# Kernel tuning notes

Hardware: AMD Instinct MI355X
Metric: run time of the kernel (lower is better)

Reference implementation:

```python
import jax, jax.numpy as jnp
import numpy as np

HID = 256      # hidden_dim
EXPAND = 2
D_INNER = HID * EXPAND
LN_EPS = 1e-5


def _gru(xs, W_ih, W_hh, b_ih, b_hh):
    """torch nn.GRU (batch_first) over axis 1. xs: (N, P, d_inner) -> (N, P, H).
    Gate order (torch): r, z, n."""
    N = xs.shape[0]
    Hd = W_hh.shape[0]
    gi = xs @ W_ih + b_ih                 # (N, P, 3H) - input gates precomputed
    gi = jnp.swapaxes(gi, 0, 1)           # (P, N, 3H) for scan over P
    h0 = jnp.zeros((N, Hd), xs.dtype)

    def step(h, gi_t):
        gh = h @ W_hh + b_hh              # (N, 3H)
        ir, iz, i_n = jnp.split(gi_t, 3, axis=-1)
        hr, hz, h_n = jnp.split(gh, 3, axis=-1)
        r = jax.nn.sigmoid(ir + hr)
        z = jax.nn.sigmoid(iz + hz)
        n = jnp.tanh(i_n + r * h_n)
        h = (1.0 - z) * n + z * h
        return h, h

    _, ys = jax.lax.scan(step, h0, gi)    # (P, N, H)
    return jnp.swapaxes(ys, 0, 1)


def _branch(x2d, lin_W, lin_b, W_ih, W_hh, b_ih, b_hh):
    # Linear -> exact GELU (torch nn.GELU default) -> GRU
    h = jax.nn.gelu(x2d @ lin_W + lin_b, approximate=False)
    return _gru(h, W_ih, W_hh, b_ih, b_hh)


def setup_inputs() -> dict:
    key = jax.random.key(0)
    ks = jax.random.split(key, 16)
    s = 0.05
    p = {
        "x": jax.random.normal(ks[0], (8, 16, 1024, HID), jnp.float32),
        "fwd_lin_W": jax.random.normal(ks[1], (HID, D_INNER)) * s,
        "fwd_lin_b": jnp.zeros((D_INNER,)),
        "fwd_W_ih": jax.random.normal(ks[2], (D_INNER, 3 * HID)) * s,
        "fwd_W_hh": jax.random.normal(ks[3], (HID, 3 * HID)) * s,
        "fwd_b_ih": jnp.zeros((3 * HID,)),
        "fwd_b_hh": jnp.zeros((3 * HID,)),
        "bwd_lin_W": jax.random.normal(ks[4], (HID, D_INNER)) * s,
        "bwd_lin_b": jnp.zeros((D_INNER,)),
        "bwd_W_ih": jax.random.normal(ks[5], (D_INNER, 3 * HID)) * s,
        "bwd_W_hh": jax.random.normal(ks[6], (HID, 3 * HID)) * s,
        "bwd_b_ih": jnp.zeros((3 * HID,)),
        "bwd_b_hh": jnp.zeros((3 * HID,)),
        "proj_W": jax.random.normal(ks[7], (2 * HID, HID)) * s,
        "proj_b": jnp.zeros((HID,)),
        "ln_g": jnp.ones((HID,)),
        "ln_b": jnp.zeros((HID,)),
    }
    return p


def reference(x, fwd_lin_W, fwd_lin_b, fwd_W_ih, fwd_W_hh, fwd_b_ih, fwd_b_hh,
              bwd_lin_W, bwd_lin_b, bwd_W_ih, bwd_W_hh, bwd_b_ih, bwd_b_hh,
              proj_W, proj_b, ln_g, ln_b):
    B, T, P, H = x.shape
    xf = x.reshape(B * T, P, H)  # every timestep gets the identical spatial pass
    f_out = _branch(xf, fwd_lin_W, fwd_lin_b, fwd_W_ih, fwd_W_hh, fwd_b_ih, fwd_b_hh)
    b_out = _branch(xf[:, ::-1], bwd_lin_W, bwd_lin_b, bwd_W_ih, bwd_W_hh, bwd_b_ih, bwd_b_hh)[:, ::-1]
    cat = jnp.concatenate([f_out, b_out], axis=-1)          # (BT, P, 2H)
    out = cat @ proj_W + proj_b                              # (BT, P, H)
    out = out.reshape(B, T, P, H) + x                        # residual
    mu = out.mean(-1, keepdims=True)
    var = out.var(-1, keepdims=True)
    return (out - mu) * jax.lax.rsqrt(var + LN_EPS) * ln_g + ln_b
```

## Files before the change

### kernel.cpp

```cpp
#include <hip/hip_runtime.h>
#include <cmath>


typedef _Float16 h8  __attribute__((ext_vector_type(8)));
typedef float    f32x4 __attribute__((ext_vector_type(4)));

#define MTOT 131072L
#define PSEQ 1024

__device__ __forceinline__ float fast_sigmoid(float x) {
    float e = __builtin_amdgcn_exp2f(-1.44269504089f * x);
    return __builtin_amdgcn_rcpf(1.f + e);
}
__device__ __forceinline__ float fast_tanh(float x) {
    float e = __builtin_amdgcn_exp2f(-2.88539008178f * x);
    return (1.f - e) * __builtin_amdgcn_rcpf(1.f + e);
}

__device__ __forceinline__ void gl_lds16(const void* g, void* lds_wave_base, int lane) {
#if defined(__has_builtin) && __has_builtin(__builtin_amdgcn_global_load_lds)
    __builtin_amdgcn_global_load_lds(
        (const __attribute__((address_space(1))) void*)g,
        (__attribute__((address_space(3))) void*)lds_wave_base, 16, 0, 0);
#else
    *((h8*)lds_wave_base + lane) = *(const h8*)g;
#endif
}

template <int MODE>
__global__ __launch_bounds__(256) void k_gemm2(
    const void* __restrict__ Aa_, const void* __restrict__ Ab_,
    const _Float16* __restrict__ Bt, const float* __restrict__ bias,
    const float* __restrict__ xres, void* __restrict__ out_, long m_off)
{
    constexpr int K   = (MODE == 0) ? 256 : 512;
    constexpr int NKT = K / 32;

    __shared__ __align__(16) _Float16 Al[128 * 32];
    __shared__ __align__(16) _Float16 Bl[128 * 32];

    const int t  = threadIdx.x;
    const int wv = t >> 6, l = t & 63;
    const int fr = l & 15, fg = l >> 4;
    const int wm = wv >> 1, wn = wv & 1;
    const long bm0 = (long)blockIdx.x * 128;
    const int  bn0 = blockIdx.y * 128;
    const int sr = t >> 2, sc = t & 3;

    f32x4 acc[4][4] = {};

    for (int kt = 0; kt < NKT; ++kt) {
        #pragma unroll
        for (int q = 0; q < 2; ++q) {
            const int r = q * 64 + sr;
            const _Float16* g = Bt + (long)(bn0 + r) * K + kt * 32 + sc * 8;
            gl_lds16(g, (char*)Bl + q * 4096 + wv * 1024, l);
        }
        if constexpr (MODE == 0) {
            #pragma unroll
            for (int q = 0; q < 2; ++q) {
                const int r = q * 64 + sr;
                const float* xs = (const float*)Aa_ + (bm0 + r) * 256 + kt * 32 + sc * 8;
                float4 v0 = *(const float4*)xs;
                float4 v1 = *(const float4*)(xs + 4);
                h8 hv;
                hv[0] = (_Float16)v0.x; hv[1] = (_Float16)v0.y;
                hv[2] = (_Float16)v0.z; hv[3] = (_Float16)v0.w;
                hv[4] = (_Float16)v1.x; hv[5] = (_Float16)v1.y;
                hv[6] = (_Float16)v1.z; hv[7] = (_Float16)v1.w;
                *(h8*)((char*)Al + r * 64 + sc * 16) = hv;
            }
        } else if constexpr (MODE == 1) {
            #pragma unroll
            for (int q = 0; q < 2; ++q) {
                const int r = q * 64 + sr;
                const _Float16* g = (const _Float16*)Aa_ + (bm0 + r) * 1024 + kt * 32 + sc * 8;
                gl_lds16(g, (char*)Al + q * 4096 + wv * 1024, l);
            }
        } else {
            const _Float16* src = (kt < 8) ? (const _Float16*)Aa_ : (const _Float16*)Ab_;
            #pragma unroll
            for (int q = 0; q < 2; ++q) {
                const int r = q * 64 + sr;
                const _Float16* g = src + (bm0 + r) * 256 + (kt & 7) * 32 + sc * 8;
                gl_lds16(g, (char*)Al + q * 4096 + wv * 1024, l);
            }
        }
        __syncthreads();

        h8 af[4], bf[4];
        #pragma unroll
        for (int fm = 0; fm < 4; ++fm)
            af[fm] = *(const h8*)((const char*)Al + (wm * 64 + fm * 16 + fr) * 64 + fg * 16);
        #pragma unroll
        for (int fn = 0; fn < 4; ++fn)
            bf[fn] = *(const h8*)((const char*)Bl + (wn * 64 + fn * 16 + fr) * 64 + fg * 16);
        #pragma unroll
        for (int fm = 0; fm < 4; ++fm)
        #pragma unroll
        for (int fn = 0; fn < 4; ++fn)
            acc[fm][fn] = __builtin_amdgcn_mfma_f32_16x16x32_f16(af[fm], bf[fn], acc[fm][fn], 0, 0, 0);
        __syncthreads();
    }

    #pragma unroll
    for (int fm = 0; fm < 4; ++fm)
    #pragma unroll
    for (int fn = 0; fn < 4; ++fn)
    #pragma unroll
    for (int r = 0; r < 4; ++r) {
        long row = bm0 + wm * 64 + fm * 16 + fg * 4 + r;
        int  col = bn0 + wn * 64 + fn * 16 + fr;
        float v = acc[fm][fn][r] + bias[col];
        if constexpr (MODE == 0) {
            v = 0.5f * v * (1.0f + erff(v * 0.70710678118654752f));
            ((_Float16*)out_)[row * 1024 + col] = (_Float16)v;
        } else if constexpr (MODE == 1) {
            long grow = row + m_off;
            int seq = (int)(grow >> 10), p = (int)(grow & 1023);
            int blk = seq >> 4, srow = seq & 15;
            int g = col >> 8, ci = col & 255;
            int wvx = ci >> 5, tp = (ci >> 4) & 1;
            int ln = (ci & 15) | ((srow >> 2) << 4);
            int e = tp * 4 + (srow & 3);
            long oidx = (((long)(blk * 1024 + p) * 3 + g) * 512 + (wvx * 64 + ln)) * 8 + e;
            ((_Float16*)out_)[oidx] = (_Float16)v;
        } else {
            v += xres[row * 256 + col];
            ((float*)out_)[row * 256 + col] = v;
        }
    }
}

__global__ __launch_bounds__(256) void k_prep_wt(
    const float* __restrict__ src, _Float16* __restrict__ dst, int Kd, int Nd)
{
    const int i = blockIdx.x * 256 + threadIdx.x;
    if (i >= Kd * Nd) return;
    const int n = i / Kd, k = i % Kd;
    dst[i] = (_Float16)src[(long)k * Nd + n];
}

__global__ __launch_bounds__(256) void k_prep_lb(
    const float* __restrict__ fb, const float* __restrict__ bb, float* __restrict__ dst)
{
    const int i = blockIdx.x * 256 + threadIdx.x;
    dst[i] = (i < 512) ? fb[i] : bb[i - 512];
}

__global__ __launch_bounds__(256) void k_prep_frag(
    const float* __restrict__ Whh, _Float16* __restrict__ Wp)
{
    const int t = blockIdx.x * 256 + threadIdx.x;
    const int l = t & 63, f = t >> 6;
    const int kt = f & 7;
    const int q  = f >> 3;
    const int tp = q & 1;
    const int q2 = q >> 1;
    const int g  = q2 % 3, w = q2 / 3;
    const int col = g * 256 + w * 32 + tp * 16 + (l & 15);
    const int k0  = kt * 32 + (l >> 4) * 8;
    h8 v;
    #pragma unroll
    for (int i = 0; i < 8; ++i)
        v[i] = (_Float16)Whh[(long)(k0 + i) * 768 + col];
    ((h8*)Wp)[t] = v;
}

__global__ __launch_bounds__(256) void k_prep_bias(
    const float* __restrict__ bih, const float* __restrict__ bhh, float* __restrict__ bc)
{
    const int c = blockIdx.x * 256 + threadIdx.x;
    bc[c] = bih[c] + (c < 512 ? bhh[c] : 0.f);
}

__global__ __launch_bounds__(512, 2) void k_gru2(
    const _Float16* __restrict__ gpf, const _Float16* __restrict__ gpb,
    const _Float16* __restrict__ Wpf, const _Float16* __restrict__ Wpb,
    const float* __restrict__ bhhf, const float* __restrict__ bhhb,
    _Float16* __restrict__ hof, _Float16* __restrict__ hob)
{
    const int b = blockIdx.x;
    const int dir = b & 1;
    const int blk = b >> 1;
    const int t = threadIdx.x;
    const int w = t >> 6, l = t & 63;
    const int lr = l & 15, lq = l >> 4;

    const _Float16* gp  = dir ? gpb : gpf;
    const _Float16* Wp  = dir ? Wpb : Wpf;
    const float*    bhh = dir ? bhhb : bhhf;
    _Float16*       hoo = dir ? hob : hof;

    __shared__ __align__(16) h8 wn_lds[8192];
    __shared__ __align__(16) _Float16 hbuf[2][16][264];

    h8 bfrz[2][2][8];
    {
        const h8* src = (const h8*)Wp + (long)w * 48 * 64 + l;
        #pragma unroll
        for (int g = 0; g < 2; ++g)
        #pragma unroll
        for (int tp = 0; tp < 2; ++tp)
        #pragma unroll
        for (int kt = 0; kt < 8; ++kt)
            bfrz[g][tp][kt] = src[((g * 2 + tp) * 8 + kt) * 64];
        #pragma unroll
        for (int tp = 0; tp < 2; ++tp)
        #pragma unroll
        for (int kt = 0; kt < 8; ++kt)
            wn_lds[((w * 2 + tp) * 8 + kt) * 64 + l] = src[((4 + tp) * 8 + kt) * 64];
    }
    const int col0 = w * 32 + lr;
    const float bn0 = bhh[512 + col0];
    const float bn1 = bhh[512 + col0 + 16];

    for (int i = t; i < 2 * 16 * 264; i += 512) ((_Float16*)hbuf)[i] = (_Float16)0.f;
    __syncthreads();

    const int d = dir ? -1 : 1;
    int p = dir ? (PSEQ - 1) : 0;
    int cur = 0;
    const long tbase = (long)t * 8;
    const long bbase = (long)blk * 1024;
    float hold[2][4] = {};

    h8 gv0 = *(const h8*)(gp + ((bbase + p) * 3 + 0) * 4096 + tbase);
    h8 gv1 = *(const h8*)(gp + ((bbase + p) * 3 + 1) * 4096 + tbase);
    h8 gv2 = *(const h8*)(gp + ((bbase + p) * 3 + 2) * 4096 + tbase);

    for (int step = 0; step < PSEQ; ++step) {
        int pn = p + d;
        pn = pn < 0 ? 0 : (pn > PSEQ - 1 ? PSEQ - 1 : pn);
        h8 nv0 = *(const h8*)(gp + ((bbase + pn) * 3 + 0) * 4096 + tbase);
        h8 nv1 = *(const h8*)(gp + ((bbase + pn) * 3 + 1) * 4096 + tbase);
        h8 nv2 = *(const h8*)(gp + ((bbase + pn) * 3 + 2) * 4096 + tbase);

        h8 af[8];
        #pragma unroll
        for (int kt = 0; kt < 8; ++kt)
            af[kt] = *(const h8*)&hbuf[cur][lr][kt * 32 + lq * 8];

        f32x4 accr[2] = {}, accz[2] = {};
        #pragma unroll
        for (int kt = 0; kt < 8; ++kt) {
            #pragma unroll
            for (int tp = 0; tp < 2; ++tp) {
                accr[tp] = __builtin_amdgcn_mfma_f32_16x16x32_f16(af[kt], bfrz[0][tp][kt], accr[tp], 0, 0, 0);
                accz[tp] = __builtin_amdgcn_mfma_f32_16x16x32_f16(af[kt], bfrz[1][tp][kt], accz[tp], 0, 0, 0);
            }
        }

        float rr[2][4], zz[2][4];
        #pragma unroll
        for (int tp = 0; tp < 2; ++tp)
        #pragma unroll
        for (int r = 0; r < 4; ++r) {
            const int e = tp * 4 + r;
            rr[tp][r] = fast_sigmoid(accr[tp][r] + (float)gv0[e]);
            zz[tp][r] = fast_sigmoid(accz[tp][r] + (float)gv1[e]);
        }

        f32x4 accn[2] = {};
        #pragma unroll
        for (int kt = 0; kt < 8; ++kt) {
            h8 bfn0 = wn_lds[((w * 2 + 0) * 8 + kt) * 64 + l];
            h8 bfn1 = wn_lds[((w * 2 + 1) * 8 + kt) * 64 + l];
            accn[0] = __builtin_amdgcn_mfma_f32_16x16x32_f16(af[kt], bfn0, accn[0], 0, 0, 0);
            accn[1] = __builtin_amdgcn_mfma_f32_16x16x32_f16(af[kt], bfn1, accn[1], 0, 0, 0);
        }

        #pragma unroll
        for (int tp = 0; tp < 2; ++tp) {
            const int col = col0 + tp * 16;
            const float bn = tp ? bn1 : bn0;
            #pragma unroll
            for (int r = 0; r < 4; ++r) {
                const int e = tp * 4 + r;
                float nh = accn[tp][r] + bn;
                float nn = fast_tanh((float)gv2[e] + rr[tp][r] * nh);
                float h  = fmaf(zz[tp][r], hold[tp][r] - nn, nn);
                hold[tp][r] = h;
                _Float16 hf = (_Float16)h;
                const int row = lq * 4 + r;
                hbuf[cur ^ 1][row][col] = hf;
                hoo[((long)(blk * 16 + row) * PSEQ + p) * 256 + col] = hf;
            }
        }
        __syncthreads();

        cur ^= 1; p += d;
        gv0 = nv0; gv1 = nv1; gv2 = nv2;
    }
}

__global__ __launch_bounds__(256) void k_ln(
    const float* __restrict__ pre, const float* __restrict__ g,
    const float* __restrict__ b, float* __restrict__ out)
{
    const long row = (long)blockIdx.x * 4 + (threadIdx.x >> 6);
    const int lane = threadIdx.x & 63;
    const float4 v = *(const float4*)&pre[row * 256 + lane * 4];
    float s  = v.x + v.y + v.z + v.w;
    float s2 = v.x * v.x + v.y * v.y + v.z * v.z + v.w * v.w;
    #pragma unroll
    for (int off = 32; off > 0; off >>= 1) {
        s  += __shfl_xor(s, off);
        s2 += __shfl_xor(s2, off);
    }
    const float mu  = s * (1.f / 256.f);
    const float var = s2 * (1.f / 256.f) - mu * mu;
    const float inv = rsqrtf(var + 1e-5f);
    const float4 gg = *(const float4*)&g[lane * 4];
    const float4 bb = *(const float4*)&b[lane * 4];
    float4 o;
    o.x = (v.x - mu) * inv * gg.x + bb.x;
    o.y = (v.y - mu) * inv * gg.y + bb.y;
    o.z = (v.z - mu) * inv * gg.z + bb.z;
    o.w = (v.w - mu) * inv * gg.w + bb.w;
    *(float4*)&out[row * 256 + lane * 4] = o;
}

extern "C" void kernel_launch(void* const* d_in, const int* in_sizes, int n_in,
                              void* d_out, int out_size, void* d_ws, size_t ws_size,
                              hipStream_t stream)
{
    const float* x       = (const float*)d_in[0];
    const float* f_lin_W = (const float*)d_in[1];
    const float* f_lin_b = (const float*)d_in[2];
    const float* f_W_ih  = (const float*)d_in[3];
    const float* f_W_hh  = (const float*)d_in[4];
    const float* f_b_ih  = (const float*)d_in[5];
    const float* f_b_hh  = (const float*)d_in[6];
    const float* b_lin_W = (const float*)d_in[7];
    const float* b_lin_b = (const float*)d_in[8];
    const float* b_W_ih  = (const float*)d_in[9];
    const float* b_W_hh  = (const float*)d_in[10];
    const float* b_b_ih  = (const float*)d_in[11];
    const float* b_b_hh  = (const float*)d_in[12];
    const float* proj_W  = (const float*)d_in[13];
    const float* proj_b  = (const float*)d_in[14];
    const float* ln_g    = (const float*)d_in[15];
    const float* ln_bb   = (const float*)d_in[16];

    char* ws = (char*)d_ws;

    size_t o = 0;
    _Float16* wt_lin  = (_Float16*)(ws + o); o += 1024 * 256 * 2;
    _Float16* wt_ihf  = (_Float16*)(ws + o); o += 768 * 512 * 2;
    _Float16* wt_ihb  = (_Float16*)(ws + o); o += 768 * 512 * 2;
    _Float16* wt_proj = (_Float16*)(ws + o); o += 256 * 512 * 2;
    float*    bl_lin  = (float*)(ws + o);    o += 1024 * 4;
    float*    bcf     = (float*)(ws + o);    o += 768 * 4;
    float*    bcb     = (float*)(ws + o);    o += 768 * 4;
    _Float16* wpf     = (_Float16*)(ws + o); o += 393216;
    _Float16* wpb     = (_Float16*)(ws + o); o += 393216;

    const size_t BASE   = 4u << 20;
    const size_t GI_PER = (size_t)MTOT * 768 * 2;
    const size_t GI_END = BASE + 2 * GI_PER;
    int chunks = 1;
    while (GI_END + (size_t)(MTOT / chunks) * 1024 * 2 > ws_size && chunks < 16)
        chunks <<= 1;
    const long MC = MTOT / chunks;

    _Float16* gif   = (_Float16*)(ws + BASE);
    _Float16* gib   = (_Float16*)(ws + BASE + GI_PER);
    float*    pre   = (float*)(ws + BASE);
    _Float16* h1cat = (_Float16*)(ws + GI_END);

    _Float16* hof = (_Float16*)d_out;
    _Float16* hob = hof + MTOT * 256;

    k_prep_wt<<<512,  256, 0, stream>>>(f_lin_W, wt_lin,             256, 512);
    k_prep_wt<<<512,  256, 0, stream>>>(b_lin_W, wt_lin + 512 * 256, 256, 512);
    k_prep_wt<<<1536, 256, 0, stream>>>(f_W_ih,  wt_ihf,             512, 768);
    k_prep_wt<<<1536, 256, 0, stream>>>(b_W_ih,  wt_ihb,             512, 768);
    k_prep_wt<<<512,  256, 0, stream>>>(proj_W,  wt_proj,            512, 256);
    k_prep_lb<<<4,    256, 0, stream>>>(f_lin_b, b_lin_b, bl_lin);
    k_prep_bias<<<3,  256, 0, stream>>>(f_b_ih, f_b_hh, bcf);
    k_prep_bias<<<3,  256, 0, stream>>>(b_b_ih, b_b_hh, bcb);
    k_prep_frag<<<96, 256, 0, stream>>>(f_W_hh, wpf);
    k_prep_frag<<<96, 256, 0, stream>>>(b_W_hh, wpb);

    for (int c = 0; c < chunks; ++c) {
        const long r0 = c * MC;
        k_gemm2<0><<<dim3(MC / 128, 8), 256, 0, stream>>>(
            x + r0 * 256, nullptr, wt_lin, bl_lin, nullptr, h1cat, 0L);
        k_gemm2<1><<<dim3(MC / 128, 6), 256, 0, stream>>>(
            h1cat, nullptr, wt_ihf, bcf, nullptr, gif, r0);
        k_gemm2<1><<<dim3(MC / 128, 6), 256, 0, stream>>>(
            h1cat + 512, nullptr, wt_ihb, bcb, nullptr, gib, r0);
    }
    k_gru2<<<16, 512, 0, stream>>>(gif, gib, wpf, wpb, f_b_hh, b_b_hh, hof, hob);
    k_gemm2<2><<<dim3(MTOT / 128, 2), 256, 0, stream>>>(
        hof, hob, wt_proj, proj_b, x, pre, 0L);
    k_ln<<<MTOT / 4, 256, 0, stream>>>(pre, ln_g, ln_bb, (float*)d_out);
}
```

Baseline: 2.528 ms.

## Stage GEMM epilogue through LDS for vectorized coalesced fp16 stores

The GELU GEMM and input-gate GEMM epilogues now write results into an LDS tile and then emit 16-byte vector stores, replacing scattered 2-byte global writes. For the gate GEMM, the block's row mapping is reordered so each tile covers 4 sequences by 32 positions. That lets whole 8-element interleaved groups be assembled in LDS and stored at once. This costs extra LDS (about 34 KB), one more barrier, and strided LDS gathers in the mode-1 transpose.

```diff
diff --git a/kernel.cpp b/kernel.cpp
--- a/kernel.cpp
+++ b/kernel.cpp
@@ -38,6 +38,7 @@
 
     __shared__ __align__(16) _Float16 Al[128 * 32];
     __shared__ __align__(16) _Float16 Bl[128 * 32];
+    __shared__ __align__(16) _Float16 Ct[(MODE == 2) ? 1 : 128][136];
 
     const int t  = threadIdx.x;
     const int wv = t >> 6, l = t & 63;
@@ -46,6 +47,9 @@
     const long bm0 = (long)blockIdx.x * 128;
     const int  bn0 = blockIdx.y * 128;
     const int sr = t >> 2, sc = t & 3;
+
+    const int grp = blockIdx.x >> 5;
+    const int pp0 = (blockIdx.x & 31) * 32;
 
     f32x4 acc[4][4] = {};
 
@@ -74,7 +78,8 @@
             #pragma unroll
             for (int q = 0; q < 2; ++q) {
                 const int r = q * 64 + sr;
-                const _Float16* g = (const _Float16*)Aa_ + (bm0 + r) * 1024 + kt * 32 + sc * 8;
+                const long lrow = (long)(grp * 4 + (r >> 5)) * 1024 + pp0 + (r & 31);
+                const _Float16* g = (const _Float16*)Aa_ + lrow * 1024 + kt * 32 + sc * 8;
                 gl_lds16(g, (char*)Al + q * 4096 + wv * 1024, l);
             }
         } else {
@@ -103,31 +108,65 @@
         __syncthreads();
     }
 
-    #pragma unroll
-    for (int fm = 0; fm < 4; ++fm)
-    #pragma unroll
-    for (int fn = 0; fn < 4; ++fn)
-    #pragma unroll
-    for (int r = 0; r < 4; ++r) {
-        long row = bm0 + wm * 64 + fm * 16 + fg * 4 + r;
-        int  col = bn0 + wn * 64 + fn * 16 + fr;
-        float v = acc[fm][fn][r] + bias[col];
+    if constexpr (MODE == 2) {
+        #pragma unroll
+        for (int fm = 0; fm < 4; ++fm)
+        #pragma unroll
+        for (int fn = 0; fn < 4; ++fn)
+        #pragma unroll
+        for (int r = 0; r < 4; ++r) {
+            long row = bm0 + wm * 64 + fm * 16 + fg * 4 + r;
+            int  col = bn0 + wn * 64 + fn * 16 + fr;
+            float v = acc[fm][fn][r] + bias[col] + xres[row * 256 + col];
+            ((float*)out_)[row * 256 + col] = v;
+        }
+    } else {
+        #pragma unroll
+        for (int fm = 0; fm < 4; ++fm)
+        #pragma unroll
+        for (int fn = 0; fn < 4; ++fn)
+        #pragma unroll
+        for (int r = 0; r < 4; ++r) {
+            int rowt = wm * 64 + fm * 16 + fg * 4 + r;
+            int colt = wn * 64 + fn * 16 + fr;
+            float v = acc[fm][fn][r] + bias[bn0 + colt];
+            if constexpr (MODE == 0)
+                v = 0.5f * v * (1.0f + erff(v * 0.70710678118654752f));
+            Ct[rowt][colt] = (_Float16)v;
+        }
+        __syncthreads();
+
         if constexpr (MODE == 0) {
-            v = 0.5f * v * (1.0f + erff(v * 0.70710678118654752f));
-            ((_Float16*)out_)[row * 1024 + col] = (_Float16)v;
-        } else if constexpr (MODE == 1) {
-            long grow = row + m_off;
-            int seq = (int)(grow >> 10), p = (int)(grow & 1023);
-            int blk = seq >> 4, srow = seq & 15;
-            int g = col >> 8, ci = col & 255;
-            int wvx = ci >> 5, tp = (ci >> 4) & 1;
-            int ln = (ci & 15) | ((srow >> 2) << 4);
-            int e = tp * 4 + (srow & 3);
-            long oidx = (((long)(blk * 1024 + p) * 3 + g) * 512 + (wvx * 64 + ln)) * 8 + e;
-            ((_Float16*)out_)[oidx] = (_Float16)v;
+            #pragma unroll
+            for (int i = 0; i < 8; ++i) {
+                const int row = i * 16 + (t >> 4);
+                const int ch  = t & 15;
+                h8 vv = *(const h8*)&Ct[row][ch * 8];
+                *(h8*)((_Float16*)out_ + (bm0 + row) * 1024 + bn0 + ch * 8) = vv;
+            }
         } else {
-            v += xres[row * 256 + col];
-            ((float*)out_)[row * 256 + col] = v;
+            const int g    = bn0 >> 8;
+            const int ci0b = (bn0 & 255) >> 5;
+            const long gseq0 = (m_off >> 10) + grp * 4;
+            const int blkg = (int)(gseq0 >> 4);
+            const int srhi = ((int)gseq0 >> 2) & 3;
+            #pragma unroll
+            for (int i = 0; i < 8; ++i) {
+                const int sid = t * 8 + i;
+                const int p_local = sid >> 6;
+                const int rem = sid & 63;
+                const int wvl = rem >> 4, lnlow = rem & 15;
+                h8 v;
+                #pragma unroll
+                for (int tp = 0; tp < 2; ++tp)
+                #pragma unroll
+                for (int s = 0; s < 4; ++s)
+                    v[tp * 4 + s] = Ct[s * 32 + p_local][wvl * 32 + tp * 16 + lnlow];
+                const long p = pp0 + p_local;
+                const long oidx = (((long)blkg * 1024 + p) * 3 + g) * 512
+                                + ((ci0b + wvl) * 64 + (srhi << 4) + lnlow);
+                *(h8*)((_Float16*)out_ + oidx * 8) = v;
+            }
         }
     }
 }
```

After: 2.402 ms. 5.0% less time.
